# Kernel tuning notes

Hardware: AMD Instinct MI355X
Metric: run time of the kernel (lower is better)

## Reference

```python
import jax, jax.numpy as jnp
import numpy as np
import math

B, Z, H, HID, T = 16384, 128, 512, 512, 32
MIN_BETA = 0.1


def setup_inputs() -> dict:
    key = jax.random.key(0)
    ks = jax.random.split(key, 8)
    # cosine beta schedule, matching torch init: (1-min)*cos(pi*(1-t)*0.5)**2 + min, t in linspace(1,0,T)
    ts = np.linspace(1.0, 0.0, T)
    beta = ((1.0 - MIN_BETA) * np.cos(math.pi * (1.0 - ts) * 0.5) ** 2 + MIN_BETA).astype(np.float32)
    s = 1.0 / np.sqrt(Z + H)
    return {
        "context_embedding": jax.random.normal(ks[0], (B, H), jnp.float32),
        "eps0": jax.random.normal(ks[1], (B, Z), jnp.float32),
        "eps": jax.random.normal(ks[2], (T, B, Z), jnp.float32),
        "beta_schedule": jnp.asarray(beta),
        "sigma0": jnp.ones((1,), jnp.float32),
        "W1": jax.random.normal(ks[3], (Z + H, HID), jnp.float32) * s,
        "b1": jnp.zeros((HID,), jnp.float32),
        "W2": jax.random.normal(ks[4], (HID, Z), jnp.float32) * (1.0 / np.sqrt(HID)),
        "b2": jnp.zeros((Z,), jnp.float32),
        "t_emb": jax.random.normal(ks[5], (T, HID), jnp.float32) * 0.02,
        "target_mu": jax.random.normal(ks[6], (B, Z), jnp.float32),
    }


def _normal_log_prob(x, mu, sigma):
    # elementwise Normal(mu, sigma).log_prob(x)
    half_log_2pi = 0.5 * jnp.log(2.0 * jnp.pi)
    return -0.5 * jnp.square((x - mu) / sigma) - jnp.log(sigma) - half_log_2pi


def reference(context_embedding, eps0, eps, beta_schedule, sigma0, W1, b1, W2, b2, t_emb, target_mu):
    num_steps = beta_schedule.shape[0]
    delta_t = 1.0 / num_steps
    sig0 = sigma0[0]

    # prior sample z_0 ~ N(0, sigma0)
    z0 = sig0 * eps0  # [B, Z]

    # backward kernel at loop index i uses beta_schedule[i-1]; i=0 wraps to beta_schedule[-1]
    beta_bwd = jnp.roll(beta_schedule, 1)

    def control(z, te):
        hid = jax.nn.relu(jnp.concatenate([z, context_embedding], axis=-1) @ W1 + b1 + te)
        return hid @ W2 + b2  # [B, Z]

    def step(carry, xs):
        z_prev, log_w = carry
        beta_f, beta_b, eps_t, te = xs
        u = control(z_prev, te)
        # forward kernel
        mu_f = z_prev + (beta_f * z_prev + u) * delta_t
        sig_f = jnp.sqrt(2.0 * beta_f * delta_t) * sig0
        z_next = mu_f + sig_f * eps_t  # rsample
        # backward kernel (evaluated at z_next)
        mu_b = z_next - beta_b * z_next * delta_t
        sig_b = jnp.sqrt(2.0 * beta_b * delta_t) * sig0
        log_w = log_w + _normal_log_prob(z_prev, mu_b, sig_b) - _normal_log_prob(z_next, mu_f, sig_f)
        return (z_next, log_w), None

    init = (z0, jnp.zeros_like(z0))
    (z_T, log_w), _ = jax.lax.scan(step, init, (beta_schedule, beta_bwd, eps, t_emb))

    # terminal + prior correction: p_z_T = N(target_mu, 1), p_z_0 = N(0, sigma0)
    log_w = log_w + _normal_log_prob(z_T, target_mu, 1.0) - _normal_log_prob(z0, 0.0, sig0)
    return jnp.sum(jnp.mean(log_w, axis=0))
```

## Files before the change

kernel.cpp:

```cpp
#include <hip/hip_runtime.h>
#include <hip/hip_bf16.h>

#define NB 16384
#define NZ 128
#define NH 512
#define NHID 512
#define NT 32

typedef __attribute__((ext_vector_type(8))) short short8;
typedef __attribute__((ext_vector_type(4))) short short4v;
typedef __attribute__((ext_vector_type(4))) float f32x4;
typedef __attribute__((ext_vector_type(2))) long long2v;

__device__ __forceinline__ short f2bf(float x) {
    union { __hip_bfloat16 h; short s; } u; u.h = __float2bfloat16(x); return u.s;
}
__device__ __forceinline__ float bf2f(short s) {
    union { unsigned int u; float f; } v; v.u = ((unsigned int)(unsigned short)s) << 16; return v.f;
}

__global__ __launch_bounds__(64) void pack_weights(const float* __restrict__ W1,
                                                   const float* __restrict__ W2,
                                                   short* __restrict__ w1aT,
                                                   long* __restrict__ w2T8,
                                                   short* __restrict__ w1bT,
                                                   float* __restrict__ out) {
    __shared__ float tile[32 * 17];
    int f = blockIdx.x;
    int l = threadIdx.x;
    int quad = l >> 4, m = l & 15;
    if (f == 0 && l == 0) *out = 0.f;

    const float* src; int ld, row0, col0;
    if (f < 128) {
        int ht = f >> 2, kt = f & 3;
        src = W1; ld = NH; row0 = kt * 32; col0 = ht * 16;
    } else if (f < 256) {
        int g = f - 128; int kt2 = g >> 3, jt = g & 7;
        src = W2; ld = NZ; row0 = kt2 * 32; col0 = jt * 16;
    } else {
        int g = f - 256; int ht = g >> 4, kt = g & 15;
        src = W1; ld = NH; row0 = 128 + kt * 32; col0 = ht * 16;
    }

    {
        int r = l >> 1, c8 = (l & 1) * 8;
        const float* p = src + (size_t)(row0 + r) * ld + col0 + c8;
        f32x4 a = *(const f32x4*)p;
        f32x4 b = *(const f32x4*)(p + 4);
#pragma unroll
        for (int j = 0; j < 4; ++j) {
            tile[r * 17 + c8 + j] = a[j];
            tile[r * 17 + c8 + 4 + j] = b[j];
        }
    }
    __syncthreads();

    float v[8];
#pragma unroll
    for (int j = 0; j < 8; ++j) v[j] = tile[(quad * 8 + j) * 17 + m];

    if (f < 128) {
        short8 o;
#pragma unroll
        for (int j = 0; j < 8; ++j) o[j] = f2bf(v[j]);
        *(short8*)(w1aT + ((size_t)f * 64 + l) * 8) = o;
    } else if (f < 256) {
        int g = f - 128;
        int lo = __builtin_amdgcn_cvt_pk_fp8_f32(v[0], v[1], 0, false);
        lo = __builtin_amdgcn_cvt_pk_fp8_f32(v[2], v[3], lo, true);
        int hi = __builtin_amdgcn_cvt_pk_fp8_f32(v[4], v[5], 0, false);
        hi = __builtin_amdgcn_cvt_pk_fp8_f32(v[6], v[7], hi, true);
        long pv = ((long)(unsigned int)hi << 32) | (unsigned int)lo;
        w2T8[(size_t)g * 64 + l] = pv;
    } else {
        int g = f - 256;
        short8 o;
#pragma unroll
        for (int j = 0; j < 8; ++j) o[j] = f2bf(v[j]);
        *(short8*)(w1bT + ((size_t)g * 64 + l) * 8) = o;
    }
}

__global__ __launch_bounds__(512, 2) void diffusion_main(
    const float* __restrict__ eps0, const float* __restrict__ eps,
    const float* __restrict__ beta, const float* __restrict__ sigma0,
    const float* __restrict__ ctx, const float* __restrict__ b1,
    const float* __restrict__ b2, const float* __restrict__ t_emb,
    const float* __restrict__ target_mu,
    const short* __restrict__ w1aT, const short* __restrict__ w1bT,
    const long* __restrict__ w2T8, float* __restrict__ out)
{
    __shared__ alignas(16) char lds[50176];
    char* zu = lds;
    char* hidb = lds + 16384;
    float* scb = (float*)(lds + 49152);
    const int w = threadIdx.x >> 6;
    const int lane = threadIdx.x & 63;
    const int quad = lane >> 4;
    const int m = lane & 15;
    const int swz = m & 7;
    const int rowbase = blockIdx.x * 64;
    const int jcol = w * 16 + quad * 4;
    const float dt = 1.0f / 32.0f;
    const float s0 = sigma0[0];
    const float logs0 = logf(s0);
    const f32x4 zero = {0.f, 0.f, 0.f, 0.f};

    const int zu_base = m * 256 + ((quad ^ swz) << 4);
    const int hw_base = m * 512 + ((quad & 1) << 2);
    const int hr_base = m * 512;
    const int zw_off  = m * 256 + ((((w << 1) + (quad >> 1)) ^ swz) << 4)
                      + ((quad & 1) << 3);

    if (threadIdx.x < 32) {
        int t = threadIdx.x;
        float bfv = beta[t];
        float bbv = beta[(t + 31) & 31];
        float sf = sqrtf(2.f * bfv * dt) * s0;
        float sb = sqrtf(2.f * bbv * dt) * s0;
        scb[t * 8 + 0] = bfv;
        scb[t * 8 + 1] = sf;
        scb[t * 8 + 2] = 1.f / sb;
        scb[t * 8 + 3] = 0.5f * (logf(bfv) - logf(bbv));
        scb[t * 8 + 4] = 1.f - bbv * dt;
    }

    f32x4 pacc[4][4];
#pragma unroll
    for (int c = 0; c < 4; ++c)
#pragma unroll
        for (int rs = 0; rs < 4; ++rs) pacc[c][rs] = zero;
#pragma unroll 4
    for (int kt = 0; kt < 16; ++kt) {
        short8 cf[4];
#pragma unroll
        for (int rs = 0; rs < 4; ++rs) {
            const float* cp = ctx + (size_t)(rowbase + rs * 16 + m) * NH + kt * 32 + quad * 8;
            f32x4 a = *(const f32x4*)cp;
            f32x4 b = *(const f32x4*)(cp + 4);
            short8 tt;
#pragma unroll
            for (int j = 0; j < 4; ++j) { tt[j] = f2bf(a[j]); tt[4 + j] = f2bf(b[j]); }
            cf[rs] = tt;
        }
#pragma unroll
        for (int c = 0; c < 4; ++c) {
            short8 af = *(const short8*)(w1bT + ((size_t)((w * 4 + c) * 16 + kt) * 64 + lane) * 8);
#pragma unroll
            for (int rs = 0; rs < 4; ++rs)
                pacc[c][rs] = __builtin_amdgcn_mfma_f32_16x16x32_bf16(af, cf[rs], pacc[c][rs], 0, 0, 0);
        }
    }
    short4v cbr[4][4];
#pragma unroll
    for (int c = 0; c < 4; ++c) {
        f32x4 bv = *(const f32x4*)(b1 + (w * 4 + c) * 16 + quad * 4);
#pragma unroll
        for (int rs = 0; rs < 4; ++rs) {
            short4v o;
#pragma unroll
            for (int i = 0; i < 4; ++i) o[i] = f2bf(pacc[c][rs][i] + bv[i]);
            cbr[c][rs] = o;
        }
    }
    f32x4 b2r = *(const f32x4*)(b2 + jcol);

    short8 wf1[4][4];
#pragma unroll
    for (int c = 0; c < 4; ++c)
#pragma unroll
        for (int kt = 0; kt < 4; ++kt)
            wf1[c][kt] = *(const short8*)(w1aT + ((size_t)((w * 4 + c) * 4 + kt) * 64 + lane) * 8);
    long wf2[16];
#pragma unroll
    for (int kt2 = 0; kt2 < 16; ++kt2)
        wf2[kt2] = w2T8[(size_t)(kt2 * 8 + w) * 64 + lane];

    float zr[4][4];
    float part = 0.f;
#pragma unroll
    for (int rs = 0; rs < 4; ++rs) {
        f32x4 e = *(const f32x4*)(eps0 + (size_t)(rowbase + rs * 16 + m) * NZ + jcol);
        short4v zb;
#pragma unroll
        for (int i = 0; i < 4; ++i) { zr[rs][i] = s0 * e[i]; zb[i] = f2bf(zr[rs][i]); }
        *(short4v*)(zu + rs * 4096 + zw_off) = zb;
    }
    __syncthreads();

#pragma unroll 1
    for (int t = 0; t < NT; ++t) {
#pragma unroll
        for (int rr = 0; rr < 2; ++rr) {
            f32x4 g1[4][2];
#pragma unroll
            for (int c = 0; c < 4; ++c)
#pragma unroll
                for (int r2 = 0; r2 < 2; ++r2) g1[c][r2] = zero;
#pragma unroll
            for (int kt = 0; kt < 4; ++kt) {
                short8 zb[2];
#pragma unroll
                for (int r2 = 0; r2 < 2; ++r2)
                    zb[r2] = *(const short8*)(zu + (rr * 2 + r2) * 4096 + (zu_base ^ (kt << 6)));
#pragma unroll
                for (int c = 0; c < 4; ++c)
#pragma unroll
                    for (int r2 = 0; r2 < 2; ++r2)
                        g1[c][r2] = __builtin_amdgcn_mfma_f32_16x16x32_bf16(
                            wf1[c][kt], zb[r2], g1[c][r2], 0, 0, 0);
            }
#pragma unroll
            for (int c = 0; c < 4; ++c) {
                int Gc = (((w * 4 + ((c & 1) << 1) + (quad >> 1)) ^ m) << 4)
                       + (((c >> 1) & 1) << 3);
                f32x4 te = *(const f32x4*)(t_emb + (size_t)t * NHID + (w * 4 + c) * 16 + quad * 4);
#pragma unroll
                for (int r2 = 0; r2 < 2; ++r2) {
                    int rs = rr * 2 + r2;
                    float p0 = fmaxf(g1[c][r2][0] + bf2f(cbr[c][rs][0]) + te[0], 0.f);
                    float p1 = fmaxf(g1[c][r2][1] + bf2f(cbr[c][rs][1]) + te[1], 0.f);
                    float p2 = fmaxf(g1[c][r2][2] + bf2f(cbr[c][rs][2]) + te[2], 0.f);
                    float p3 = fmaxf(g1[c][r2][3] + bf2f(cbr[c][rs][3]) + te[3], 0.f);
                    int pk = __builtin_amdgcn_cvt_pk_fp8_f32(p0, p1, 0, false);
                    pk = __builtin_amdgcn_cvt_pk_fp8_f32(p2, p3, pk, true);
                    *(int*)(hidb + rs * 8192 + hw_base + Gc) = pk;
                }
            }
        }
        __syncthreads();

        f32x4 ef[4];
        {
            const float* ept = eps + (size_t)t * NB * NZ + (size_t)rowbase * NZ + jcol;
#pragma unroll
            for (int rs = 0; rs < 4; ++rs)
                ef[rs] = *(const f32x4*)(ept + (size_t)(rs * 16 + m) * NZ);
        }
        f32x4 sca = *(const f32x4*)(scb + t * 8);
        float c1mb = scb[t * 8 + 4];

        f32x4 ua[4];
#pragma unroll
        for (int rs = 0; rs < 4; ++rs) ua[rs] = zero;
#pragma unroll
        for (int kp = 0; kp < 8; ++kp) {
            long wlo = wf2[kp * 2];
            long whi = wf2[kp * 2 + 1];
            int go = ((kp * 4 + quad) ^ m) << 4;
#pragma unroll
            for (int rs = 0; rs < 4; ++rs) {
                long2v h2 = *(const long2v*)(hidb + rs * 8192 + hr_base + go);
                ua[rs] = __builtin_amdgcn_mfma_f32_16x16x32_fp8_fp8(wlo, h2[0], ua[rs], 0, 0, 0);
                ua[rs] = __builtin_amdgcn_mfma_f32_16x16x32_fp8_fp8(whi, h2[1], ua[rs], 0, 0, 0);
            }
        }

#pragma unroll
        for (int rs = 0; rs < 4; ++rs) {
            short4v zb;
#pragma unroll
            for (int i = 0; i < 4; ++i) {
                float z = zr[rs][i];
                float e = ef[rs][i];
                float uu = ua[rs][i] + b2r[i];
                float mu_f = z + (sca[0] * z + uu) * dt;
                float zn = mu_f + sca[1] * e;
                float d = (z - zn * c1mb) * sca[2];
                part += -0.5f * d * d + 0.5f * e * e + sca[3];
                zr[rs][i] = zn;
                zb[i] = f2bf(zn);
            }
            *(short4v*)(zu + rs * 4096 + zw_off) = zb;
        }
        __syncthreads();
    }

#pragma unroll
    for (int rs = 0; rs < 4; ++rs) {
        const float* ep = eps0 + (size_t)(rowbase + rs * 16 + m) * NZ + jcol;
        const float* tp = target_mu + (size_t)(rowbase + rs * 16 + m) * NZ + jcol;
        f32x4 a = *(const f32x4*)ep;
        f32x4 ta = *(const f32x4*)tp;
#pragma unroll
        for (int i = 0; i < 4; ++i) {
            float d0 = zr[rs][i] - ta[i];
            part += -0.5f * d0 * d0 + 0.5f * a[i] * a[i] + logs0;
        }
    }
#pragma unroll
    for (int off = 32; off >= 1; off >>= 1) part += __shfl_xor(part, off, 64);
    if (lane == 0) atomicAdd(out, part * (1.0f / NB));
}

extern "C" void kernel_launch(void* const* d_in, const int* in_sizes, int n_in,
                              void* d_out, int out_size, void* d_ws, size_t ws_size,
                              hipStream_t stream) {
    const float* ctx  = (const float*)d_in[0];
    const float* eps0 = (const float*)d_in[1];
    const float* eps  = (const float*)d_in[2];
    const float* beta = (const float*)d_in[3];
    const float* sig0 = (const float*)d_in[4];
    const float* W1   = (const float*)d_in[5];
    const float* b1   = (const float*)d_in[6];
    const float* W2   = (const float*)d_in[7];
    const float* b2   = (const float*)d_in[8];
    const float* temb = (const float*)d_in[9];
    const float* tmu  = (const float*)d_in[10];
    float* out = (float*)d_out;

    char* ws = (char*)d_ws;
    short* w1aT = (short*)ws;
    long*  w2T8 = (long*)(ws + 131072);
    short* w1bT = (short*)(ws + 196608);

    pack_weights<<<768, 64, 0, stream>>>(W1, W2, w1aT, w2T8, w1bT, out);
    diffusion_main<<<256, 512, 0, stream>>>(eps0, eps, beta, sig0, ctx, b1, b2,
                                            temb, tmu, w1aT, w1bT, w2T8, out);
}
```

Baseline: 526.6 us.

## Double waves per block to 16 and stage context-bias tiles in LDS

Each block now runs 1024 threads (16 waves) instead of 512. Every wave owns two hidden tiles instead of four in the first GEMM and a half row-slice in the second GEMM. The precomputed context projection plus bias, previously held in registers, is written to LDS and reread each step, which frees VGPRs. The intent is more waves per CU to hide MFMA and LDS latency across the serial timestep loop. In exchange LDS use grows to about 113KB, each 1024-thread barrier gets more expensive, and the hidden loop runs un-unrolled.

```diff
diff --git a/kernel.cpp b/kernel.cpp
--- a/kernel.cpp
+++ b/kernel.cpp
@@ -82,7 +82,7 @@
     }
 }
 
-__global__ __launch_bounds__(512, 2) void diffusion_main(
+__global__ __launch_bounds__(1024, 1) void diffusion_main(
     const float* __restrict__ eps0, const float* __restrict__ eps,
     const float* __restrict__ beta, const float* __restrict__ sigma0,
     const float* __restrict__ ctx, const float* __restrict__ b1,
@@ -91,17 +91,20 @@
     const short* __restrict__ w1aT, const short* __restrict__ w1bT,
     const long* __restrict__ w2T8, float* __restrict__ out)
 {
-    __shared__ alignas(16) char lds[50176];
+    __shared__ alignas(16) char lds[115712];
     char* zu = lds;
     char* hidb = lds + 16384;
     float* scb = (float*)(lds + 49152);
+    char* cbl = lds + 50176;
     const int w = threadIdx.x >> 6;
     const int lane = threadIdx.x & 63;
     const int quad = lane >> 4;
     const int m = lane & 15;
     const int swz = m & 7;
     const int rowbase = blockIdx.x * 64;
-    const int jcol = w * 16 + quad * 4;
+    const int jt = w & 7;
+    const int rp = w >> 3;
+    const int jcol = jt * 16 + quad * 4;
     const float dt = 1.0f / 32.0f;
     const float s0 = sigma0[0];
     const float logs0 = logf(s0);
@@ -110,7 +113,7 @@
     const int zu_base = m * 256 + ((quad ^ swz) << 4);
     const int hw_base = m * 512 + ((quad & 1) << 2);
     const int hr_base = m * 512;
-    const int zw_off  = m * 256 + ((((w << 1) + (quad >> 1)) ^ swz) << 4)
+    const int zw_off  = m * 256 + ((((jt << 1) + (quad >> 1)) ^ swz) << 4)
                       + ((quad & 1) << 3);
 
     if (threadIdx.x < 32) {
@@ -126,150 +129,144 @@
         scb[t * 8 + 4] = 1.f - bbv * dt;
     }
 
-    f32x4 pacc[4][4];
-#pragma unroll
-    for (int c = 0; c < 4; ++c)
-#pragma unroll
-        for (int rs = 0; rs < 4; ++rs) pacc[c][rs] = zero;
+    {
+        f32x4 pacc[2][4];
+#pragma unroll
+        for (int c = 0; c < 2; ++c)
+#pragma unroll
+            for (int rs = 0; rs < 4; ++rs) pacc[c][rs] = zero;
 #pragma unroll 4
-    for (int kt = 0; kt < 16; ++kt) {
-        short8 cf[4];
-#pragma unroll
-        for (int rs = 0; rs < 4; ++rs) {
-            const float* cp = ctx + (size_t)(rowbase + rs * 16 + m) * NH + kt * 32 + quad * 8;
-            f32x4 a = *(const f32x4*)cp;
-            f32x4 b = *(const f32x4*)(cp + 4);
-            short8 tt;
-#pragma unroll
-            for (int j = 0; j < 4; ++j) { tt[j] = f2bf(a[j]); tt[4 + j] = f2bf(b[j]); }
-            cf[rs] = tt;
-        }
-#pragma unroll
-        for (int c = 0; c < 4; ++c) {
-            short8 af = *(const short8*)(w1bT + ((size_t)((w * 4 + c) * 16 + kt) * 64 + lane) * 8);
-#pragma unroll
-            for (int rs = 0; rs < 4; ++rs)
-                pacc[c][rs] = __builtin_amdgcn_mfma_f32_16x16x32_bf16(af, cf[rs], pacc[c][rs], 0, 0, 0);
-        }
-    }
-    short4v cbr[4][4];
-#pragma unroll
-    for (int c = 0; c < 4; ++c) {
-        f32x4 bv = *(const f32x4*)(b1 + (w * 4 + c) * 16 + quad * 4);
-#pragma unroll
-        for (int rs = 0; rs < 4; ++rs) {
-            short4v o;
-#pragma unroll
-            for (int i = 0; i < 4; ++i) o[i] = f2bf(pacc[c][rs][i] + bv[i]);
-            cbr[c][rs] = o;
+        for (int kt = 0; kt < 16; ++kt) {
+            short8 cf[4];
+#pragma unroll
+            for (int rs = 0; rs < 4; ++rs) {
+                const float* cp = ctx + (size_t)(rowbase + rs * 16 + m) * NH + kt * 32 + quad * 8;
+                f32x4 a = *(const f32x4*)cp;
+                f32x4 b = *(const f32x4*)(cp + 4);
+                short8 tt;
+#pragma unroll
+                for (int j = 0; j < 4; ++j) { tt[j] = f2bf(a[j]); tt[4 + j] = f2bf(b[j]); }
+                cf[rs] = tt;
+            }
+#pragma unroll
+            for (int c = 0; c < 2; ++c) {
+                short8 af = *(const short8*)(w1bT + ((size_t)((2 * w + c) * 16 + kt) * 64 + lane) * 8);
+#pragma unroll
+                for (int rs = 0; rs < 4; ++rs)
+                    pacc[c][rs] = __builtin_amdgcn_mfma_f32_16x16x32_bf16(af, cf[rs], pacc[c][rs], 0, 0, 0);
+            }
+        }
+#pragma unroll
+        for (int c = 0; c < 2; ++c) {
+            int ht = 2 * w + c;
+            f32x4 bv = *(const f32x4*)(b1 + ht * 16 + quad * 4);
+#pragma unroll
+            for (int rs = 0; rs < 4; ++rs) {
+                short4v o;
+#pragma unroll
+                for (int i = 0; i < 4; ++i) o[i] = f2bf(pacc[c][rs][i] + bv[i]);
+                *(short4v*)(cbl + ((ht * 4 + rs) * 64 + lane) * 8) = o;
+            }
         }
     }
     f32x4 b2r = *(const f32x4*)(b2 + jcol);
 
-    short8 wf1[4][4];
-#pragma unroll
-    for (int c = 0; c < 4; ++c)
+    short8 wf1[2][4];
+#pragma unroll
+    for (int c = 0; c < 2; ++c)
 #pragma unroll
         for (int kt = 0; kt < 4; ++kt)
-            wf1[c][kt] = *(const short8*)(w1aT + ((size_t)((w * 4 + c) * 4 + kt) * 64 + lane) * 8);
+            wf1[c][kt] = *(const short8*)(w1aT + ((size_t)((2 * w + c) * 4 + kt) * 64 + lane) * 8);
     long wf2[16];
 #pragma unroll
     for (int kt2 = 0; kt2 < 16; ++kt2)
-        wf2[kt2] = w2T8[(size_t)(kt2 * 8 + w) * 64 + lane];
-
-    float zr[4][4];
+        wf2[kt2] = w2T8[(size_t)(kt2 * 8 + jt) * 64 + lane];
+
+    const float* ep0 = eps + (size_t)(rowbase + (2 * rp) * 16 + m) * NZ + jcol;
+
+    float zr[2][4];
     float part = 0.f;
 #pragma unroll
-    for (int rs = 0; rs < 4; ++rs) {
+    for (int r2 = 0; r2 < 2; ++r2) {
+        int rs = 2 * rp + r2;
         f32x4 e = *(const f32x4*)(eps0 + (size_t)(rowbase + rs * 16 + m) * NZ + jcol);
         short4v zb;
 #pragma unroll
-        for (int i = 0; i < 4; ++i) { zr[rs][i] = s0 * e[i]; zb[i] = f2bf(zr[rs][i]); }
+        for (int i = 0; i < 4; ++i) { zr[r2][i] = s0 * e[i]; zb[i] = f2bf(zr[r2][i]); }
         *(short4v*)(zu + rs * 4096 + zw_off) = zb;
     }
     __syncthreads();
 
 #pragma unroll 1
     for (int t = 0; t < NT; ++t) {
-#pragma unroll
-        for (int rr = 0; rr < 2; ++rr) {
-            f32x4 g1[4][2];
-#pragma unroll
-            for (int c = 0; c < 4; ++c)
-#pragma unroll
-                for (int r2 = 0; r2 < 2; ++r2) g1[c][r2] = zero;
+#pragma unroll 1
+        for (int rr = 0; rr < 4; ++rr) {
+            f32x4 g1[2];
+            g1[0] = zero; g1[1] = zero;
 #pragma unroll
             for (int kt = 0; kt < 4; ++kt) {
-                short8 zb[2];
-#pragma unroll
-                for (int r2 = 0; r2 < 2; ++r2)
-                    zb[r2] = *(const short8*)(zu + (rr * 2 + r2) * 4096 + (zu_base ^ (kt << 6)));
-#pragma unroll
-                for (int c = 0; c < 4; ++c)
-#pragma unroll
-                    for (int r2 = 0; r2 < 2; ++r2)
-                        g1[c][r2] = __builtin_amdgcn_mfma_f32_16x16x32_bf16(
-                            wf1[c][kt], zb[r2], g1[c][r2], 0, 0, 0);
-            }
-#pragma unroll
-            for (int c = 0; c < 4; ++c) {
-                int Gc = (((w * 4 + ((c & 1) << 1) + (quad >> 1)) ^ m) << 4)
-                       + (((c >> 1) & 1) << 3);
-                f32x4 te = *(const f32x4*)(t_emb + (size_t)t * NHID + (w * 4 + c) * 16 + quad * 4);
-#pragma unroll
-                for (int r2 = 0; r2 < 2; ++r2) {
-                    int rs = rr * 2 + r2;
-                    float p0 = fmaxf(g1[c][r2][0] + bf2f(cbr[c][rs][0]) + te[0], 0.f);
-                    float p1 = fmaxf(g1[c][r2][1] + bf2f(cbr[c][rs][1]) + te[1], 0.f);
-                    float p2 = fmaxf(g1[c][r2][2] + bf2f(cbr[c][rs][2]) + te[2], 0.f);
-                    float p3 = fmaxf(g1[c][r2][3] + bf2f(cbr[c][rs][3]) + te[3], 0.f);
-                    int pk = __builtin_amdgcn_cvt_pk_fp8_f32(p0, p1, 0, false);
-                    pk = __builtin_amdgcn_cvt_pk_fp8_f32(p2, p3, pk, true);
-                    *(int*)(hidb + rs * 8192 + hw_base + Gc) = pk;
-                }
+                short8 zb = *(const short8*)(zu + rr * 4096 + (zu_base ^ (kt << 6)));
+                g1[0] = __builtin_amdgcn_mfma_f32_16x16x32_bf16(wf1[0][kt], zb, g1[0], 0, 0, 0);
+                g1[1] = __builtin_amdgcn_mfma_f32_16x16x32_bf16(wf1[1][kt], zb, g1[1], 0, 0, 0);
+            }
+#pragma unroll
+            for (int c = 0; c < 2; ++c) {
+                int ht = 2 * w + c;
+                int wo = ht >> 2, co = ht & 3;
+                int Gc = (((wo * 4 + ((co & 1) << 1) + (quad >> 1)) ^ m) << 4)
+                       + (((co >> 1) & 1) << 3);
+                f32x4 te = *(const f32x4*)(t_emb + (size_t)t * NHID + ht * 16 + quad * 4);
+                short4v cbv = *(const short4v*)(cbl + ((ht * 4 + rr) * 64 + lane) * 8);
+                float p0 = fmaxf(g1[c][0] + bf2f(cbv[0]) + te[0], 0.f);
+                float p1 = fmaxf(g1[c][1] + bf2f(cbv[1]) + te[1], 0.f);
+                float p2 = fmaxf(g1[c][2] + bf2f(cbv[2]) + te[2], 0.f);
+                float p3 = fmaxf(g1[c][3] + bf2f(cbv[3]) + te[3], 0.f);
+                int pk = __builtin_amdgcn_cvt_pk_fp8_f32(p0, p1, 0, false);
+                pk = __builtin_amdgcn_cvt_pk_fp8_f32(p2, p3, pk, true);
+                *(int*)(hidb + rr * 8192 + hw_base + Gc) = pk;
             }
         }
         __syncthreads();
 
-        f32x4 ef[4];
+        f32x4 ef[2];
         {
-            const float* ept = eps + (size_t)t * NB * NZ + (size_t)rowbase * NZ + jcol;
-#pragma unroll
-            for (int rs = 0; rs < 4; ++rs)
-                ef[rs] = *(const f32x4*)(ept + (size_t)(rs * 16 + m) * NZ);
+            const float* ept = ep0 + (size_t)t * NB * NZ;
+            ef[0] = *(const f32x4*)ept;
+            ef[1] = *(const f32x4*)(ept + 16 * NZ);
         }
         f32x4 sca = *(const f32x4*)(scb + t * 8);
         float c1mb = scb[t * 8 + 4];
 
-        f32x4 ua[4];
-#pragma unroll
-        for (int rs = 0; rs < 4; ++rs) ua[rs] = zero;
+        f32x4 ua[2];
+        ua[0] = zero; ua[1] = zero;
 #pragma unroll
         for (int kp = 0; kp < 8; ++kp) {
             long wlo = wf2[kp * 2];
             long whi = wf2[kp * 2 + 1];
             int go = ((kp * 4 + quad) ^ m) << 4;
 #pragma unroll
-            for (int rs = 0; rs < 4; ++rs) {
+            for (int r2 = 0; r2 < 2; ++r2) {
+                int rs = 2 * rp + r2;
                 long2v h2 = *(const long2v*)(hidb + rs * 8192 + hr_base + go);
-                ua[rs] = __builtin_amdgcn_mfma_f32_16x16x32_fp8_fp8(wlo, h2[0], ua[rs], 0, 0, 0);
-                ua[rs] = __builtin_amdgcn_mfma_f32_16x16x32_fp8_fp8(whi, h2[1], ua[rs], 0, 0, 0);
-            }
-        }
-
-#pragma unroll
-        for (int rs = 0; rs < 4; ++rs) {
+                ua[r2] = __builtin_amdgcn_mfma_f32_16x16x32_fp8_fp8(wlo, h2[0], ua[r2], 0, 0, 0);
+                ua[r2] = __builtin_amdgcn_mfma_f32_16x16x32_fp8_fp8(whi, h2[1], ua[r2], 0, 0, 0);
+            }
+        }
+
+#pragma unroll
+        for (int r2 = 0; r2 < 2; ++r2) {
+            int rs = 2 * rp + r2;
             short4v zb;
 #pragma unroll
             for (int i = 0; i < 4; ++i) {
-                float z = zr[rs][i];
-                float e = ef[rs][i];
-                float uu = ua[rs][i] + b2r[i];
+                float z = zr[r2][i];
+                float e = ef[r2][i];
+                float uu = ua[r2][i] + b2r[i];
                 float mu_f = z + (sca[0] * z + uu) * dt;
                 float zn = mu_f + sca[1] * e;
                 float d = (z - zn * c1mb) * sca[2];
                 part += -0.5f * d * d + 0.5f * e * e + sca[3];
-                zr[rs][i] = zn;
+                zr[r2][i] = zn;
                 zb[i] = f2bf(zn);
             }
             *(short4v*)(zu + rs * 4096 + zw_off) = zb;
@@ -278,14 +275,15 @@
     }
 
 #pragma unroll
-    for (int rs = 0; rs < 4; ++rs) {
+    for (int r2 = 0; r2 < 2; ++r2) {
+        int rs = 2 * rp + r2;
         const float* ep = eps0 + (size_t)(rowbase + rs * 16 + m) * NZ + jcol;
         const float* tp = target_mu + (size_t)(rowbase + rs * 16 + m) * NZ + jcol;
         f32x4 a = *(const f32x4*)ep;
         f32x4 ta = *(const f32x4*)tp;
 #pragma unroll
         for (int i = 0; i < 4; ++i) {
-            float d0 = zr[rs][i] - ta[i];
+            float d0 = zr[r2][i] - ta[i];
             part += -0.5f * d0 * d0 + 0.5f * a[i] * a[i] + logs0;
         }
     }
@@ -316,6 +314,6 @@
     short* w1bT = (short*)(ws + 196608);
 
     pack_weights<<<768, 64, 0, stream>>>(W1, W2, w1aT, w2T8, w1bT, out);
-    diffusion_main<<<256, 512, 0, stream>>>(eps0, eps, beta, sig0, ctx, b1, b2,
-                                            temb, tmu, w1aT, w1bT, w2T8, out);
-}
+    diffusion_main<<<256, 1024, 0, stream>>>(eps0, eps, beta, sig0, ctx, b1, b2,
+                                             temb, tmu, w1aT, w1bT, w2T8, out);
+}
```

Result: slower. 563.4 us (+7.0%).
